# Performance work log

Hardware: AMD Instinct MI355X
Metric: run time of the kernel (lower is better)

Reference implementation:

```python
import jax, jax.numpy as jnp
import numpy as np
import math

NUM_HEADS = 8
EPS = 1e-5
LEAKY_SLOPE = 0.01


def _attention(q, k, v, mask):
    # q:[S,64] k,v:[T,64] -> [S,64]; scale by sqrt(d) per source (q.shape[1])
    s = (q @ k.T) / math.sqrt(q.shape[1])
    if mask:
        S, T = s.shape
        tri = jnp.tril(jnp.ones((S, T), dtype=bool))
        s = jnp.where(tri, s, -jnp.inf)
    return jax.nn.softmax(s, axis=1) @ v


def _mha(q, k, v, w_o, mask):
    # all heads share the same (q,k,v) in the source, so cat over heads == tile
    head = _attention(q, k, v, mask)            # [S,64]
    concat = jnp.tile(head, (1, NUM_HEADS))     # [S,512]
    return concat @ w_o


def _layernorm(x, g, b):
    mu = jnp.mean(x, axis=-1, keepdims=True)
    var = jnp.var(x, axis=-1, keepdims=True)
    return (x - mu) * jax.lax.rsqrt(var + EPS) * g + b


def setup_inputs() -> dict:
    key = jax.random.key(0)
    ks = jax.random.split(key, 12)
    S, D, P, H = 8192, 512, 64, 2048
    sd = 1.0 / math.sqrt(D)
    return {
        "encoder_output": jax.random.normal(ks[0], (S, D), jnp.float32),
        "previous_stage_output": jax.random.normal(ks[1], (S, D), jnp.float32),
        "wq_m": jax.random.normal(ks[2], (D, P), jnp.float32) * sd,
        "wk_m": jax.random.normal(ks[3], (D, P), jnp.float32) * sd,
        "wv_m": jax.random.normal(ks[4], (D, P), jnp.float32) * sd,
        "wq_c": jax.random.normal(ks[5], (D, P), jnp.float32) * sd,
        "wk_c": jax.random.normal(ks[6], (D, P), jnp.float32) * sd,
        "wv_c": jax.random.normal(ks[7], (D, P), jnp.float32) * sd,
        "w_o": jax.random.normal(ks[8], (D, D), jnp.float32) * sd,
        "ln_g": jnp.ones((D,), jnp.float32),
        "ln_b": jnp.zeros((D,), jnp.float32),
        "w1": jax.random.normal(ks[9], (D, H), jnp.float32) * sd,
        "b1": jnp.zeros((H,), jnp.float32),
        "w2": jax.random.normal(ks[10], (H, D), jnp.float32) * (1.0 / math.sqrt(H)),
        "b2": jnp.zeros((D,), jnp.float32),
    }


def reference(encoder_output, previous_stage_output, wq_m, wk_m, wv_m,
              wq_c, wk_c, wv_c, w_o, ln_g, ln_b, w1, b1, w2, b2):
    prev = previous_stage_output
    # masked (causal) self-attention over previous decoder output
    masked_mh = _mha(prev @ wq_m, prev @ wk_m, prev @ wv_m, w_o, mask=True)
    # cross attention: q from masked output, k/v from encoder output
    mh = _mha(masked_mh @ wq_c, encoder_output @ wk_c, encoder_output @ wv_c,
              w_o, mask=False)
    x = _layernorm(mh + prev, ln_g, ln_b)
    h = x @ w1 + b1
    h = jnp.where(h >= 0, h, LEAKY_SLOPE * h)
    ffn = h @ w2 + b2
    out = _layernorm(ffn + x, ln_g, ln_b)
    return (encoder_output, out)
```

## Files before the change

### kernel.cpp

```cpp
#include <hip/hip_runtime.h>
#include <hip/hip_bf16.h>

typedef unsigned short u16;
typedef __attribute__((ext_vector_type(4))) float f32x4;
typedef __attribute__((ext_vector_type(8))) __bf16 bf16x8;
typedef __attribute__((ext_vector_type(8))) short short8;
typedef __attribute__((ext_vector_type(4))) short s16x4;

constexpr int SEQ = 8192;
constexpr int DM  = 512;
constexpr int HD  = 64;
constexpr int HFF = 2048;

__device__ __forceinline__ float b2f(u16 u){
  union { unsigned int i; float f; } v; v.i = ((unsigned int)u) << 16; return v.f;
}
__device__ __forceinline__ u16 f2b(float f){
  union { float f; unsigned int i; } v; v.f = f;
  unsigned int r = v.i + 0x7FFFu + ((v.i >> 16) & 1u);
  return (u16)(r >> 16);
}

__device__ __forceinline__ void gload16(const u16* g, u16* lds){
  __builtin_amdgcn_global_load_lds(
      (const __attribute__((address_space(1))) void*)g,
      (__attribute__((address_space(3))) void*)lds, 16, 0, 0);
}

__global__ __launch_bounds__(256) void copycvt_k(const float* __restrict__ in,
                                                 float* __restrict__ outf,
                                                 u16* __restrict__ outb, long n8){
  long i = blockIdx.x * 256L + threadIdx.x;
  if(i >= n8) return;
  f32x4 a = ((const f32x4*)in)[i*2];
  f32x4 b = ((const f32x4*)in)[i*2+1];
  ((f32x4*)outf)[i*2]   = a;
  ((f32x4*)outf)[i*2+1] = b;
  u16 ov[8];
  for(int j=0;j<4;j++){ ov[j] = f2b(a[j]); ov[4+j] = f2b(b[j]); }
  ((short8*)outb)[i] = *(short8*)ov;
}

__global__ __launch_bounds__(256) void cvt_k(const float* __restrict__ in,
                                             u16* __restrict__ out, long n8){
  long i = blockIdx.x * 256L + threadIdx.x;
  if(i >= n8) return;
  f32x4 a = ((const f32x4*)in)[i*2];
  f32x4 b = ((const f32x4*)in)[i*2+1];
  u16 ov[8];
  for(int j=0;j<4;j++){ ov[j] = f2b(a[j]); ov[4+j] = f2b(b[j]); }
  ((short8*)out)[i] = *(short8*)ov;
}

__global__ __launch_bounds__(256) void wtrans6_k(const float* __restrict__ w0,
                                                 const float* __restrict__ w1,
                                                 const float* __restrict__ w2,
                                                 const float* __restrict__ w3,
                                                 const float* __restrict__ w4,
                                                 const float* __restrict__ w5,
                                                 u16* __restrict__ out){
  __shared__ u16 t[32][33];
  const float* ins[6] = {w0,w1,w2,w3,w4,w5};
  const float* in = ins[blockIdx.z];
  u16* o = out + (long)blockIdx.z * 32768;
  int c0 = blockIdx.x*32, r0 = blockIdx.y*32;
  int tx = threadIdx.x, ty = threadIdx.y;
  for(int i=0;i<4;i++)
    t[ty+i*8][tx] = f2b(in[(long)(r0+ty+i*8)*HD + c0+tx]);
  __syncthreads();
  for(int i=0;i<4;i++) o[(long)(c0+ty+i*8)*DM + r0+tx] = t[tx][ty+i*8];
}

template<int IN_F>
__global__ __launch_bounds__(256) void transpose_k(const void* __restrict__ inp,
                                                   u16* __restrict__ out, int R, int C){
  __shared__ u16 t[32][33];
  int c0 = blockIdx.x*32, r0 = blockIdx.y*32;
  int tx = threadIdx.x, ty = threadIdx.y;
  for(int i=0;i<4;i++){
    long idx = (long)(r0+ty+i*8)*C + c0+tx;
    u16 v;
    if constexpr (IN_F) v = f2b(((const float*)inp)[idx]);
    else                v = ((const u16*)inp)[idx];
    t[ty+i*8][tx] = v;
  }
  __syncthreads();
  for(int i=0;i<4;i++) out[(long)(c0+ty+i*8)*R + r0+tx] = t[tx][ty+i*8];
}

__global__ __launch_bounds__(256) void vtrans2_k(const u16* __restrict__ v0,
                                                 u16* __restrict__ o0,
                                                 const u16* __restrict__ v1,
                                                 u16* __restrict__ o1){
  __shared__ u16 t[32][33];
  const u16* in = blockIdx.z ? v1 : v0;
  u16* o = blockIdx.z ? o1 : o0;
  int c0 = blockIdx.x*32, r0 = blockIdx.y*32;
  int tx = threadIdx.x, ty = threadIdx.y;
  for(int i=0;i<4;i++) t[ty+i*8][tx] = in[(long)(r0+ty+i*8)*HD + c0+tx];
  __syncthreads();
  for(int i=0;i<4;i++) o[(long)(c0+ty+i*8)*SEQ + r0+tx] = t[tx][ty+i*8];
}

__global__ __launch_bounds__(256) void wosum_k(const float* __restrict__ wo,
                                               u16* __restrict__ outT){
  int tid = blockIdx.x*256 + threadIdx.x;
  int n = tid >> 6, p = tid & 63;
  float s = 0.f;
  for(int h=0; h<8; h++) s += wo[(long)(h*64+p)*DM + n];
  outT[n*64+p] = f2b(s);
}

template<bool WRITE_BF>
__global__ __launch_bounds__(256) void add_ln(const u16* __restrict__ Xa,
                                              const float* __restrict__ Xb,
                                              const float* __restrict__ G,
                                              const float* __restrict__ Bb,
                                              float* __restrict__ OutF,
                                              u16* __restrict__ OutB){
  int row  = blockIdx.x*4 + (threadIdx.x>>6);
  int lane = threadIdx.x & 63;
  short8 a8 = *(const short8*)&Xa[(long)row*DM + lane*8];
  f32x4 b0 = *(const f32x4*)&Xb[(long)row*DM + lane*8];
  f32x4 b1 = *(const f32x4*)&Xb[(long)row*DM + lane*8 + 4];
  float x[8]; float s=0.f, s2=0.f;
  for(int i=0;i<8;i++){
    float bv = (i<4) ? b0[i] : b1[i-4];
    x[i] = b2f((u16)a8[i]) + bv;
    s += x[i]; s2 += x[i]*x[i];
  }
  for(int o=1;o<64;o<<=1){ s += __shfl_xor(s,o); s2 += __shfl_xor(s2,o); }
  float mu  = s * (1.f/DM);
  float var = s2 * (1.f/DM) - mu*mu;
  float rstd = rsqrtf(var + 1e-5f);
  f32x4 g0 = *(const f32x4*)&G[lane*8];
  f32x4 g1 = *(const f32x4*)&G[lane*8+4];
  f32x4 p0 = *(const f32x4*)&Bb[lane*8];
  f32x4 p1 = *(const f32x4*)&Bb[lane*8+4];
  float of[8]; u16 ob[8];
  for(int i=0;i<8;i++){
    float gv = (i<4)?g0[i]:g1[i-4], bv2 = (i<4)?p0[i]:p1[i-4];
    float v = (x[i]-mu)*rstd*gv + bv2;
    of[i] = v; ob[i] = f2b(v);
  }
  *(f32x4*)&OutF[(long)row*DM + lane*8]     = *(f32x4*)&of[0];
  *(f32x4*)&OutF[(long)row*DM + lane*8 + 4] = *(f32x4*)&of[4];
  if constexpr (WRITE_BF)
    *(short8*)&OutB[(long)row*DM + lane*8] = *(short8*)ob;
}

template<int BM,int BN,int EPI>
__global__ __launch_bounds__(256) void gemm2(const u16* __restrict__ A,
                                             const u16* __restrict__ Bt,
                                             u16* __restrict__ C,
                                             const float* __restrict__ bias,
                                             int N, int K, long sB, long sC){
  constexpr int WR=2, WC=2;
  constexpr int WM = BM/WR, WN = BN/WC;
  constexpr int MF = WM/16, NF = WN/16;
  __shared__ u16 As[2][BM*64];
  __shared__ u16 Bs[2][BN*64];

  const int tid = threadIdx.x;
  const int wid = tid >> 6, lane = tid & 63;
  const int g = lane >> 4, lr = lane & 15;
  const int m0 = blockIdx.x * BM;
  const int n0 = blockIdx.y * BN;
  Bt += (long)blockIdx.z * sB;
  C  += (long)blockIdx.z * sC;
  const int wr = wid / WC, wc = wid % WC;

  f32x4 acc[MF][NF];
  for(int m=0;m<MF;m++) for(int n=0;n<NF;n++) acc[m][n] = (f32x4)0.f;

  auto stage = [&](const u16* src, int base_row, u16* lds, int rows, int k0){
    const int cpw = rows/32;
    for(int i=0;i<cpw;i++){
      int chunk = wid*cpw + i;
      int Lb = chunk*1024;
      int L  = Lb + lane*16;
      int row = L >> 7, cb = L & 127;
      int scb = cb ^ ((row&7)<<4);
      gload16(&src[(long)(base_row+row)*K + k0 + (scb>>1)], lds + (Lb>>1));
    }
  };

  const int nk = K/64;
  stage(A, m0, As[0], BM, 0);
  stage(Bt, n0, Bs[0], BN, 0);
  __syncthreads();
  int cur = 0;
  for(int t=0;t<nk;t++){
    if(t+1<nk){
      stage(A, m0, As[cur^1], BM, (t+1)*64);
      stage(Bt, n0, Bs[cur^1], BN, (t+1)*64);
    }
    for(int kc=0;kc<2;kc++){
      const int co = (kc*32 + g*8) ^ ((lr&7)<<3);
      bf16x8 af[MF], bfr[NF];
      for(int m=0;m<MF;m++) af[m]  = *(const bf16x8*)&As[cur][(wr*WM+m*16+lr)*64 + co];
      for(int n=0;n<NF;n++) bfr[n] = *(const bf16x8*)&Bs[cur][(wc*WN+n*16+lr)*64 + co];
      for(int m=0;m<MF;m++)
        for(int n=0;n<NF;n++)
          acc[m][n] = __builtin_amdgcn_mfma_f32_16x16x32_bf16(af[m], bfr[n], acc[m][n], 0,0,0);
    }
    __syncthreads();
    cur ^= 1;
  }
  for(int m=0;m<MF;m++){
    int row = m0 + wr*WM + m*16 + g*4;
    for(int n=0;n<NF;n++){
      int col = n0 + wc*WN + n*16 + lr;
      float bv = 0.f;
      if constexpr (EPI>=1) bv = bias[col];
      for(int j=0;j<4;j++){
        float v = acc[m][n][j] + bv;
        if constexpr (EPI==2) v = (v >= 0.f) ? v : 0.01f*v;
        C[(long)(row+j)*N + col] = f2b(v);
      }
    }
  }
}

template<bool CAUSAL>
__global__ __launch_bounds__(256) void attn_part_k(const u16* __restrict__ Q,
                                                   const u16* __restrict__ Km,
                                                   const u16* __restrict__ Vt,
                                                   float* __restrict__ Op,
                                                   float* __restrict__ Ml){
  constexpr int LDK = 72;
  constexpr int NCH = 16;
  constexpr int CTI = 8;
  __shared__ u16 Ks[64*LDK];
  __shared__ u16 Vs[64*LDK];
  __shared__ u16 Ps[4*16*LDK];

  const int qb = blockIdx.x, ci = blockIdx.y;
  if(CAUSAL && ci*CTI > qb) return;

  const int tid = threadIdx.x, wid = tid>>6, lane = tid&63;
  const int g = lane>>4, lr = lane&15, r4 = g*4;
  const int qrow = qb*64 + wid*16;

  bf16x8 qf[2];
  for(int kc=0;kc<2;kc++){
    bf16x8 t = *(const bf16x8*)&Q[(long)(qrow + lr)*HD + kc*32 + g*8];
    for(int i=0;i<8;i++) t[i] = (__bf16)((float)t[i] * 0.1803368801f);
    qf[kc] = t;
  }

  f32x4 o[4]; for(int n=0;n<4;n++) o[n] = (f32x4)0.f;
  float mst = -1e30f, lst = 0.f;

  const int tdiag = qb - ci*CTI;
  const int tmax = CAUSAL ? min(CTI, tdiag + 1) : CTI;

  const int sr0 = tid>>3, sc0 = (tid&7)*8;
  short8 rK0, rK1, rV0, rV1;
  {
    const int kv0 = ci*512;
    rK0 = *(const short8*)&Km[(long)(kv0+sr0)*HD + sc0];
    rK1 = *(const short8*)&Km[(long)(kv0+sr0+32)*HD + sc0];
    rV0 = *(const short8*)&Vt[(long)sr0*SEQ + kv0 + sc0];
    rV1 = *(const short8*)&Vt[(long)(sr0+32)*SEQ + kv0 + sc0];
  }

  for(int t=0; t<tmax; ++t){
    const int kv0 = ci*512 + t*64;
    __syncthreads();
    *(short8*)&Ks[sr0*LDK + sc0]      = rK0;
    *(short8*)&Ks[(sr0+32)*LDK + sc0] = rK1;
    *(short8*)&Vs[sr0*LDK + sc0]      = rV0;
    *(short8*)&Vs[(sr0+32)*LDK + sc0] = rV1;
    __syncthreads();
    if(t+1 < tmax){
      const int kn = kv0 + 64;
      rK0 = *(const short8*)&Km[(long)(kn+sr0)*HD + sc0];
      rK1 = *(const short8*)&Km[(long)(kn+sr0+32)*HD + sc0];
      rV0 = *(const short8*)&Vt[(long)sr0*SEQ + kn + sc0];
      rV1 = *(const short8*)&Vt[(long)(sr0+32)*SEQ + kn + sc0];
    }

    f32x4 s[4]; for(int n=0;n<4;n++) s[n] = (f32x4)0.f;
    for(int kc=0;kc<2;kc++){
      for(int n=0;n<4;n++){
        bf16x8 kf = *(const bf16x8*)&Ks[(n*16+lr)*LDK + kc*32 + g*8];
        s[n] = __builtin_amdgcn_mfma_f32_16x16x32_bf16(kf, qf[kc], s[n], 0,0,0);
      }
    }
    if(CAUSAL && t == tdiag){
      int row = qrow + lr;
      for(int n=0;n<4;n++)
        for(int j=0;j<4;j++)
          if(kv0 + n*16 + r4 + j > row) s[n][j] = -1e30f;
    }
    float pmax = s[0][0];
    for(int n=0;n<4;n++)
      for(int j=0;j<4;j++) pmax = fmaxf(pmax, s[n][j]);
    pmax = fmaxf(pmax, __shfl_xor(pmax,16));
    pmax = fmaxf(pmax, __shfl_xor(pmax,32));
    if(__any(pmax > mst + 8.f)){
      float mn = fmaxf(mst, pmax);
      float fac = exp2f(mst - mn);
      mst = mn; lst *= fac;
      float fj0 = __shfl(fac, r4+0), fj1 = __shfl(fac, r4+1);
      float fj2 = __shfl(fac, r4+2), fj3 = __shfl(fac, r4+3);
      for(int n=0;n<4;n++){
        o[n][0] *= fj0; o[n][1] *= fj1; o[n][2] *= fj2; o[n][3] *= fj3;
      }
    }
    float rs = 0.f;
    for(int n=0;n<4;n++){
      u16 w[4];
      for(int j=0;j<4;j++){
        float p = exp2f(s[n][j] - mst);
        rs += p;
        __bf16 pb = (__bf16)p;
        union { __bf16 b; u16 u; } cv; cv.b = pb;
        w[j] = cv.u;
      }
      *(s16x4*)&Ps[(wid*16 + lr)*LDK + n*16 + r4] = *(s16x4*)w;
    }
    rs += __shfl_xor(rs,16); rs += __shfl_xor(rs,32);
    lst += rs;
    for(int kc=0;kc<2;kc++){
      bf16x8 pf = *(const bf16x8*)&Ps[(wid*16 + lr)*LDK + kc*32 + g*8];
      for(int n=0;n<4;n++){
        bf16x8 vf = *(const bf16x8*)&Vs[(n*16+lr)*LDK + kc*32 + g*8];
        o[n] = __builtin_amdgcn_mfma_f32_16x16x32_bf16(pf, vf, o[n], 0,0,0);
      }
    }
  }
  const long pr = (long)(qb*NCH + ci)*64;
  for(int n=0;n<4;n++)
    for(int j=0;j<4;j++)
      Op[(pr + wid*16 + r4 + j)*64 + n*16 + lr] = o[n][j];
  if(lane < 16){
    Ml[(pr + wid*16 + lr)*2]     = mst;
    Ml[(pr + wid*16 + lr)*2 + 1] = lst;
  }
}

template<bool CAUSAL>
__global__ __launch_bounds__(256) void attn_red_k(const float* __restrict__ Op,
                                                  const float* __restrict__ Ml,
                                                  u16* __restrict__ O){
  int r = blockIdx.x*4 + (threadIdx.x>>6);
  int d = threadIdx.x & 63;
  int qb = r >> 6, rt = r & 63;
  int nch = CAUSAL ? (qb>>3) + 1 : 16;
  long base = (long)qb*16*64 + rt;
  float m = -1e30f;
  for(int i=0;i<nch;i++) m = fmaxf(m, Ml[(base + i*64)*2]);
  float L = 0.f, acc = 0.f;
  for(int i=0;i<nch;i++){
    float mi = Ml[(base + i*64)*2], li = Ml[(base + i*64)*2 + 1];
    float w = exp2f(mi - m);
    L   += li * w;
    acc += w * Op[(base + i*64)*64 + d];
  }
  O[(long)r*HD + d] = f2b(acc / L);
}

extern "C" void kernel_launch(void* const* d_in, const int* in_sizes, int n_in,
                              void* d_out, int out_size, void* d_ws, size_t ws_size,
                              hipStream_t stream){
  const float* enc  = (const float*)d_in[0];
  const float* prev = (const float*)d_in[1];
  const float* wq_m = (const float*)d_in[2];
  const float* wk_m = (const float*)d_in[3];
  const float* wv_m = (const float*)d_in[4];
  const float* wq_c = (const float*)d_in[5];
  const float* wk_c = (const float*)d_in[6];
  const float* wv_c = (const float*)d_in[7];
  const float* w_o  = (const float*)d_in[8];
  const float* ln_g = (const float*)d_in[9];
  const float* ln_b = (const float*)d_in[10];
  const float* w1   = (const float*)d_in[11];
  const float* b1   = (const float*)d_in[12];
  const float* w2   = (const float*)d_in[13];
  const float* b2   = (const float*)d_in[14];
  float* out = (float*)d_out;
  u16* ws  = (u16*)d_ws;

  u16* wq_m_t = ws;
  u16* wk_c_t = wq_m_t + 4*32768;
  u16* wost   = wq_m_t + 6*32768;
  u16* w1_t   = wost   + 32768;
  u16* w2_t   = w1_t   + 1048576;
  u16* enc_b  = w2_t   + 1048576;
  u16* prev_b = enc_b  + 4194304;
  u16* q_m    = prev_b + 4194304;
  u16* k_m    = q_m    + 524288;
  u16* v_m    = k_m    + 524288;
  u16* v_m_t  = v_m    + 524288;
  u16* head_m = v_m_t  + 524288;
  u16* k_c    = head_m + 524288;
  u16* v_c    = k_c    + 524288;
  u16* v_c_t  = v_c    + 524288;
  u16* q_c    = v_c_t  + 524288;
  u16* head_c = q_c    + 524288;
  u16* mmh    = head_c + 524288;
  u16* mh     = mmh    + 4194304;
  u16* xb     = mh     + 4194304;
  float* xf   = (float*)(xb + 4194304);
  u16* hbuf   = enc_b;
  u16* ffn    = mh;
  float* Op   = (float*)mmh;
  float* Ml   = Op + (long)128*16*64*64;

  dim3 b256(256), tb(32,8);

  copycvt_k<<<dim3(2048), b256, 0, stream>>>(enc, out, enc_b, (long)SEQ*DM/8);
  cvt_k<<<dim3(2048), b256, 0, stream>>>(prev, prev_b, (long)SEQ*DM/8);

  wtrans6_k<<<dim3(2,16,6), tb, 0, stream>>>(wq_m, wk_m, wv_m, wq_c, wk_c, wv_c, wq_m_t);
  transpose_k<1><<<dim3(64,16), tb, 0, stream>>>(w1, w1_t, DM, HFF);
  transpose_k<1><<<dim3(16,64), tb, 0, stream>>>(w2, w2_t, HFF, DM);
  wosum_k<<<dim3(128), b256, 0, stream>>>(w_o, wost);

  gemm2<64,64,0><<<dim3(SEQ/64,1,3), b256, 0, stream>>>(prev_b, wq_m_t, q_m, nullptr, HD, DM, 32768, 524288);
  gemm2<64,64,0><<<dim3(SEQ/64,1,2), b256, 0, stream>>>(enc_b,  wk_c_t, k_c, nullptr, HD, DM, 32768, 524288);
  vtrans2_k<<<dim3(2,256,2), tb, 0, stream>>>(v_m, v_m_t, v_c, v_c_t);

  attn_part_k<true><<<dim3(SEQ/64, 16), b256, 0, stream>>>(q_m, k_m, v_m_t, Op, Ml);
  attn_red_k<true><<<dim3(SEQ/4), b256, 0, stream>>>(Op, Ml, head_m);
  gemm2<64,128,0><<<dim3(SEQ/64,4,1), b256, 0, stream>>>(head_m, wost, mmh, nullptr, DM, HD, 0, 0);

  gemm2<64,64,0><<<dim3(SEQ/64,1,1), b256, 0, stream>>>(mmh, wq_m_t + 3*32768, q_c, nullptr, HD, DM, 0, 0);
  attn_part_k<false><<<dim3(SEQ/64, 16), b256, 0, stream>>>(q_c, k_c, v_c_t, Op, Ml);
  attn_red_k<false><<<dim3(SEQ/4), b256, 0, stream>>>(Op, Ml, head_c);
  gemm2<64,128,0><<<dim3(SEQ/64,4,1), b256, 0, stream>>>(head_c, wost, mh, nullptr, DM, HD, 0, 0);

  add_ln<true><<<dim3(SEQ/4), b256, 0, stream>>>(mh, prev, ln_g, ln_b, xf, xb);

  gemm2<128,128,2><<<dim3(SEQ/128,HFF/128,1), b256, 0, stream>>>(xb, w1_t, hbuf, b1, HFF, DM, 0, 0);
  gemm2<64,128,1><<<dim3(SEQ/64,4,1),         b256, 0, stream>>>(hbuf, w2_t, ffn, b2, DM, HFF, 0, 0);

  add_ln<false><<<dim3(SEQ/4), b256, 0, stream>>>(ffn, xf, ln_g, ln_b, out + (long)SEQ*DM, nullptr);
}
```

Baseline: 224.2 us.

## Double-buffer attention K/V tiles via async global-to-LDS loads with XOR swizzle

The split-KV attention kernel now stages K and V tiles straight into LDS with global_load_lds into two buffers, prefetching the next tile while the current one is computed. This replaces the register-staged copy that needed two barriers per iteration. An XOR swizzle on the unpadded 64-wide rows replaces the padding that avoided bank conflicts. It uses twice the K/V LDS and depends on the swizzle being consistent between writes and reads.

```diff
diff --git a/kernel.cpp b/kernel.cpp
--- a/kernel.cpp
+++ b/kernel.cpp
@@ -228,12 +228,12 @@
                                                    const u16* __restrict__ Vt,
                                                    float* __restrict__ Op,
                                                    float* __restrict__ Ml){
-  constexpr int LDK = 72;
+  constexpr int LDP = 72;
   constexpr int NCH = 16;
   constexpr int CTI = 8;
-  __shared__ u16 Ks[64*LDK];
-  __shared__ u16 Vs[64*LDK];
-  __shared__ u16 Ps[4*16*LDK];
+  __shared__ u16 Ks[2][64*64];
+  __shared__ u16 Vs[2][64*64];
+  __shared__ u16 Ps[4*16*LDP];
 
   const int qb = blockIdx.x, ci = blockIdx.y;
   if(CAUSAL && ci*CTI > qb) return;
@@ -241,6 +241,19 @@
   const int tid = threadIdx.x, wid = tid>>6, lane = tid&63;
   const int g = lane>>4, lr = lane&15, r4 = g*4;
   const int qrow = qb*64 + wid*16;
+
+  const int srow0 = wid*16 + (lane>>3);
+  const int scb   = ((lane&7)*16) ^ (((lane>>3)&7)<<4);
+  const int sco   = scb>>1;
+
+  auto stageKV = [&](int buf, int kv0){
+    for(int i=0;i<2;i++){
+      int Lb  = (wid*2+i)*1024;
+      int row = srow0 + i*8;
+      gload16(&Km[(long)(kv0+row)*HD + sco],     &Ks[buf][Lb>>1]);
+      gload16(&Vt[(long)row*SEQ + kv0 + sco],    &Vs[buf][Lb>>1]);
+    }
+  };
 
   bf16x8 qf[2];
   for(int kc=0;kc<2;kc++){
@@ -255,36 +268,19 @@
   const int tdiag = qb - ci*CTI;
   const int tmax = CAUSAL ? min(CTI, tdiag + 1) : CTI;
 
-  const int sr0 = tid>>3, sc0 = (tid&7)*8;
-  short8 rK0, rK1, rV0, rV1;
-  {
-    const int kv0 = ci*512;
-    rK0 = *(const short8*)&Km[(long)(kv0+sr0)*HD + sc0];
-    rK1 = *(const short8*)&Km[(long)(kv0+sr0+32)*HD + sc0];
-    rV0 = *(const short8*)&Vt[(long)sr0*SEQ + kv0 + sc0];
-    rV1 = *(const short8*)&Vt[(long)(sr0+32)*SEQ + kv0 + sc0];
-  }
+  stageKV(0, ci*512);
+  __syncthreads();
+  int cur = 0;
 
   for(int t=0; t<tmax; ++t){
     const int kv0 = ci*512 + t*64;
-    __syncthreads();
-    *(short8*)&Ks[sr0*LDK + sc0]      = rK0;
-    *(short8*)&Ks[(sr0+32)*LDK + sc0] = rK1;
-    *(short8*)&Vs[sr0*LDK + sc0]      = rV0;
-    *(short8*)&Vs[(sr0+32)*LDK + sc0] = rV1;
-    __syncthreads();
-    if(t+1 < tmax){
-      const int kn = kv0 + 64;
-      rK0 = *(const short8*)&Km[(long)(kn+sr0)*HD + sc0];
-      rK1 = *(const short8*)&Km[(long)(kn+sr0+32)*HD + sc0];
-      rV0 = *(const short8*)&Vt[(long)sr0*SEQ + kn + sc0];
-      rV1 = *(const short8*)&Vt[(long)(sr0+32)*SEQ + kn + sc0];
-    }
+    if(t+1 < tmax) stageKV(cur^1, kv0 + 64);
 
     f32x4 s[4]; for(int n=0;n<4;n++) s[n] = (f32x4)0.f;
     for(int kc=0;kc<2;kc++){
+      const int co = (kc*32 + g*8) ^ ((lr&7)<<3);
       for(int n=0;n<4;n++){
-        bf16x8 kf = *(const bf16x8*)&Ks[(n*16+lr)*LDK + kc*32 + g*8];
+        bf16x8 kf = *(const bf16x8*)&Ks[cur][(n*16+lr)*64 + co];
         s[n] = __builtin_amdgcn_mfma_f32_16x16x32_bf16(kf, qf[kc], s[n], 0,0,0);
       }
     }
@@ -319,17 +315,20 @@
         union { __bf16 b; u16 u; } cv; cv.b = pb;
         w[j] = cv.u;
       }
-      *(s16x4*)&Ps[(wid*16 + lr)*LDK + n*16 + r4] = *(s16x4*)w;
+      *(s16x4*)&Ps[(wid*16 + lr)*LDP + n*16 + r4] = *(s16x4*)w;
     }
     rs += __shfl_xor(rs,16); rs += __shfl_xor(rs,32);
     lst += rs;
     for(int kc=0;kc<2;kc++){
-      bf16x8 pf = *(const bf16x8*)&Ps[(wid*16 + lr)*LDK + kc*32 + g*8];
+      bf16x8 pf = *(const bf16x8*)&Ps[(wid*16 + lr)*LDP + kc*32 + g*8];
+      const int co = (kc*32 + g*8) ^ ((lr&7)<<3);
       for(int n=0;n<4;n++){
-        bf16x8 vf = *(const bf16x8*)&Vs[(n*16+lr)*LDK + kc*32 + g*8];
+        bf16x8 vf = *(const bf16x8*)&Vs[cur][(n*16+lr)*64 + co];
         o[n] = __builtin_amdgcn_mfma_f32_16x16x32_bf16(pf, vf, o[n], 0,0,0);
       }
     }
+    __syncthreads();
+    cur ^= 1;
   }
   const long pr = (long)(qb*NCH + ci)*64;
   for(int n=0;n<4;n++)
```

Result: no change. 228.0 us (+1.7%).
